# Performance work log

Measured on AMD Instinct MI355X. Metric: run time of the kernel, lower is better.

## Reference

```python
import jax, jax.numpy as jnp
import numpy as np

H = 128

def setup_inputs() -> dict:
    key = jax.random.key(0)
    ks = jax.random.split(key, 7)
    x = jax.random.normal(ks[0], (4, 65536, H), dtype=jnp.float32)
    # Linear(3H -> H) and Linear(H -> H), torch-style fan-in init scale
    W1 = jax.random.normal(ks[1], (3 * H, H), dtype=jnp.float32) / np.sqrt(3 * H)
    b1 = jax.random.normal(ks[2], (H,), dtype=jnp.float32) * 0.01
    W2 = jax.random.normal(ks[3], (H, H), dtype=jnp.float32) / np.sqrt(H)
    b2 = jax.random.normal(ks[4], (H,), dtype=jnp.float32) * 0.01
    gamma = jnp.ones((H,), dtype=jnp.float32)
    beta = jnp.zeros((H,), dtype=jnp.float32)
    return {"x": x, "W1": W1, "b1": b1, "W2": W2, "b2": b2, "gamma": gamma, "beta": beta}


def _layernorm(h, gamma, beta, eps=1e-5):
    mu = jnp.mean(h, axis=-1, keepdims=True)
    var = jnp.var(h, axis=-1, keepdims=True)
    return (h - mu) * jax.lax.rsqrt(var + eps) * gamma + beta


def reference(x, W1, b1, W2, b2, gamma, beta):
    # circular neighbor gather along node dim
    prev_x = jnp.roll(x, 1, axis=1)
    next_x = jnp.roll(x, -1, axis=1)
    cat = jnp.concatenate([prev_x, x, next_x], axis=-1)  # [B, N, 3H]
    h = jax.nn.relu(jnp.einsum('bnc,ch->bnh', cat, W1) + b1)
    delta = jnp.einsum('bnh,hk->bnk', h, W2) + b2
    return jax.nn.relu(_layernorm(x + delta, gamma, beta))
```

## Files before the change

### kernel.cpp

```cpp
#include <hip/hip_runtime.h>


typedef __bf16 bf16x8 __attribute__((ext_vector_type(8)));
typedef __bf16 bf16x4 __attribute__((ext_vector_type(4)));
typedef float  f32x4  __attribute__((ext_vector_type(4)));

#define H      128
#define NB     65536
#define TILE   64
#define XS     136
#define HSS    136
#define VS     132
#define NTILES 4096

__global__ __launch_bounds__(256, 2)
void cbb_kernel(const float* __restrict__ x, const float* __restrict__ W1,
                const float* __restrict__ b1, const float* __restrict__ W2,
                const float* __restrict__ b2, const float* __restrict__ gamma,
                const float* __restrict__ beta, float* __restrict__ out) {
    __shared__ __align__(16) char raw[(66 * XS + 64 * HSS) * 2];
    __bf16* xs = (__bf16*)raw;
    __bf16* hs = xs + 66 * XS;
    float*  vs = (float*)raw;
    __shared__ float s_mu[64], s_rs[64], s_gamma[128], s_beta[128];

    const int tid  = threadIdx.x;
    const int wid  = tid >> 6;
    const int lane = tid & 63;
    const int l    = lane & 15;
    const int g    = lane >> 4;
    const int col0 = wid * 32;
    const int c0   = col0 + l;
    const int c1   = col0 + 16 + l;

    if (tid < 128) { s_gamma[tid] = gamma[tid]; s_beta[tid] = beta[tid]; }

    const float b1r0 = b1[c0], b1r1 = b1[c1];
    const float b2r0 = b2[c0], b2r1 = b2[c1];

    bf16x8 w1f[12][2];
#pragma unroll
    for (int ks = 0; ks < 12; ++ks) {
#pragma unroll
        for (int ct = 0; ct < 2; ++ct) {
            const int cc = col0 + ct * 16 + l;
            bf16x8 f;
#pragma unroll
            for (int j = 0; j < 8; ++j)
                f[j] = (__bf16)W1[(ks * 32 + g * 8 + j) * H + cc];
            w1f[ks][ct] = f;
        }
    }
    bf16x8 w2f[4][2];
#pragma unroll
    for (int ks = 0; ks < 4; ++ks) {
#pragma unroll
        for (int ct = 0; ct < 2; ++ct) {
            const int cc = col0 + ct * 16 + l;
            bf16x8 f;
#pragma unroll
            for (int j = 0; j < 8; ++j)
                f[j] = (__bf16)W2[(ks * 32 + g * 8 + j) * H + cc];
            w2f[ks][ct] = f;
        }
    }

    for (int t = blockIdx.x; t < NTILES; t += gridDim.x) {
        const int b  = t >> 10;
        const int n0 = (t & 1023) << 6;
        const size_t rowbase = (size_t)b * NB;

        __syncthreads();

        for (int q = tid; q < 66 * 32; q += 256) {
            const int r = q >> 5, c = q & 31;
            const int grow = (n0 - 1 + r + NB) & (NB - 1);
            const float4 f = *(const float4*)(x + ((rowbase + grow) * H + c * 4));
            bf16x4 v4;
            v4[0] = (__bf16)f.x; v4[1] = (__bf16)f.y;
            v4[2] = (__bf16)f.z; v4[3] = (__bf16)f.w;
            *(bf16x4*)(xs + r * XS + c * 4) = v4;
        }
        __syncthreads();

        f32x4 acc[4][2];
#pragma unroll
        for (int rt = 0; rt < 4; ++rt)
#pragma unroll
            for (int ct = 0; ct < 2; ++ct)
                acc[rt][ct] = (f32x4){0.f, 0.f, 0.f, 0.f};

#pragma unroll
        for (int rt = 0; rt < 4; ++rt) {
            const int rb = rt * 16 + l;
#pragma unroll
            for (int ks = 0; ks < 12; ++ks) {
                const int k = ks * 32 + g * 8;
                const bf16x8 a = *(const bf16x8*)(xs + (rb + (k >> 7)) * XS + (k & 127));
                acc[rt][0] = __builtin_amdgcn_mfma_f32_16x16x32_bf16(a, w1f[ks][0], acc[rt][0], 0, 0, 0);
                acc[rt][1] = __builtin_amdgcn_mfma_f32_16x16x32_bf16(a, w1f[ks][1], acc[rt][1], 0, 0, 0);
            }
        }

#pragma unroll
        for (int rt = 0; rt < 4; ++rt) {
#pragma unroll
            for (int i = 0; i < 4; ++i) {
                const int row = rt * 16 + g * 4 + i;
                hs[row * HSS + c0] = (__bf16)fmaxf(acc[rt][0][i] + b1r0, 0.f);
                hs[row * HSS + c1] = (__bf16)fmaxf(acc[rt][1][i] + b1r1, 0.f);
            }
        }
        __syncthreads();

        f32x4 acc2[4][2];
#pragma unroll
        for (int rt = 0; rt < 4; ++rt)
#pragma unroll
            for (int ct = 0; ct < 2; ++ct)
                acc2[rt][ct] = (f32x4){0.f, 0.f, 0.f, 0.f};

#pragma unroll
        for (int rt = 0; rt < 4; ++rt) {
            const int rb = rt * 16 + l;
#pragma unroll
            for (int ks = 0; ks < 4; ++ks) {
                const bf16x8 a = *(const bf16x8*)(hs + rb * HSS + ks * 32 + g * 8);
                acc2[rt][0] = __builtin_amdgcn_mfma_f32_16x16x32_bf16(a, w2f[ks][0], acc2[rt][0], 0, 0, 0);
                acc2[rt][1] = __builtin_amdgcn_mfma_f32_16x16x32_bf16(a, w2f[ks][1], acc2[rt][1], 0, 0, 0);
            }
        }

#pragma unroll
        for (int rt = 0; rt < 4; ++rt) {
#pragma unroll
            for (int i = 0; i < 4; ++i) {
                const int row = rt * 16 + g * 4 + i;
                acc2[rt][0][i] += b2r0 + (float)xs[(row + 1) * XS + c0];
                acc2[rt][1][i] += b2r1 + (float)xs[(row + 1) * XS + c1];
            }
        }
        __syncthreads();

#pragma unroll
        for (int rt = 0; rt < 4; ++rt) {
#pragma unroll
            for (int i = 0; i < 4; ++i) {
                const int row = rt * 16 + g * 4 + i;
                vs[row * VS + c0] = acc2[rt][0][i];
                vs[row * VS + c1] = acc2[rt][1][i];
            }
        }
        __syncthreads();

        {
            const int row = tid >> 2;
            const int cb  = (tid & 3) * 32;
            float s = 0.f, qq = 0.f;
#pragma unroll
            for (int c8 = 0; c8 < 8; ++c8) {
                const f32x4 vv = *(const f32x4*)(vs + row * VS + cb + c8 * 4);
#pragma unroll
                for (int e = 0; e < 4; ++e) { s += vv[e]; qq += vv[e] * vv[e]; }
            }
            s  += __shfl_xor(s, 1, 4);  s  += __shfl_xor(s, 2, 4);
            qq += __shfl_xor(qq, 1, 4); qq += __shfl_xor(qq, 2, 4);
            const float muv = s * (1.f / 128.f);
            const float var = qq * (1.f / 128.f) - muv * muv;
            if ((tid & 3) == 0) { s_mu[row] = muv; s_rs[row] = rsqrtf(var + 1e-5f); }
        }
        __syncthreads();

        {
            const int row = tid >> 2;
            const int cb  = (tid & 3) * 32;
            const float muv = s_mu[row], rv = s_rs[row];
            float* op = out + (rowbase + n0 + row) * H + cb;
#pragma unroll
            for (int c8 = 0; c8 < 8; ++c8) {
                const f32x4 vv = *(const f32x4*)(vs + row * VS + cb + c8 * 4);
                const f32x4 gm = *(const f32x4*)(s_gamma + cb + c8 * 4);
                const f32x4 bt = *(const f32x4*)(s_beta + cb + c8 * 4);
                f32x4 o;
#pragma unroll
                for (int e = 0; e < 4; ++e)
                    o[e] = fmaxf((vv[e] - muv) * rv * gm[e] + bt[e], 0.f);
                *(f32x4*)(op + c8 * 4) = o;
            }
        }
    }
}

extern "C" void kernel_launch(void* const* d_in, const int* in_sizes, int n_in,
                              void* d_out, int out_size, void* d_ws, size_t ws_size,
                              hipStream_t stream) {
    const float* x     = (const float*)d_in[0];
    const float* W1    = (const float*)d_in[1];
    const float* b1    = (const float*)d_in[2];
    const float* W2    = (const float*)d_in[3];
    const float* b2    = (const float*)d_in[4];
    const float* gamma = (const float*)d_in[5];
    const float* beta  = (const float*)d_in[6];
    float* out = (float*)d_out;

    cbb_kernel<<<512, 256, 0, stream>>>(x, W1, b1, W2, b2, gamma, beta, out);
}
```

Measured before the change: 296.6 us.

## Restructure kernel into per-wave row chunks with shared-memory weights and register-only epilogue

Weights move from per-thread registers into shared memory, laid out in MFMA fragment order and shared by 16 waves in a 1024-thread block. Each wave now handles 16-row chunks on its own. It computes the transposed product (W as the A operand), reads x directly from global memory with software prefetch, and passes the hidden activations between GEMMs through lane shuffles instead of LDS. LayerNorm is done in registers with cross-lane shuffles, which removes every per-tile __syncthreads and the LDS staging. In exchange, the neighbouring x rows are reloaded from global memory (about 3x reads, likely served by cache), weights are read from LDS on every MFMA, and occupancy is one block per CU.

Result: slower. 998.0 us (+236.5%).

```diff
diff --git a/kernel.cpp b/kernel.cpp
--- a/kernel.cpp
+++ b/kernel.cpp
@@ -2,191 +2,180 @@
 
 
 typedef __bf16 bf16x8 __attribute__((ext_vector_type(8)));
-typedef __bf16 bf16x4 __attribute__((ext_vector_type(4)));
 typedef float  f32x4  __attribute__((ext_vector_type(4)));
 
 #define H      128
 #define NB     65536
-#define TILE   64
-#define XS     136
-#define HSS    136
-#define VS     132
-#define NTILES 4096
+#define BLK    1024
+#define GRID   256
+#define RPW    64
+#define CHUNK  16
 
-__global__ __launch_bounds__(256, 2)
+union U8 { bf16x8 v; unsigned u[4]; };
+
+static __device__ __forceinline__ unsigned pkbf(float a, float b) {
+    union { __bf16 h; unsigned short u; } ua, ub;
+    ua.h = (__bf16)a; ub.h = (__bf16)b;
+    return ((unsigned)ub.u << 16) | (unsigned)ua.u;
+}
+
+__global__ __launch_bounds__(BLK, 1)
 void cbb_kernel(const float* __restrict__ x, const float* __restrict__ W1,
                 const float* __restrict__ b1, const float* __restrict__ W2,
                 const float* __restrict__ b2, const float* __restrict__ gamma,
                 const float* __restrict__ beta, float* __restrict__ out) {
-    __shared__ __align__(16) char raw[(66 * XS + 64 * HSS) * 2];
-    __bf16* xs = (__bf16*)raw;
-    __bf16* hs = xs + 66 * XS;
-    float*  vs = (float*)raw;
-    __shared__ float s_mu[64], s_rs[64], s_gamma[128], s_beta[128];
+    __shared__ __align__(16) __bf16 w1s[12 * 8 * 512];
+    __shared__ __align__(16) __bf16 w2s[4 * 8 * 512];
+    __shared__ __align__(16) float s_b1[128], s_b2[128], s_gamma[128], s_beta[128];
 
     const int tid  = threadIdx.x;
     const int wid  = tid >> 6;
     const int lane = tid & 63;
     const int l    = lane & 15;
     const int g    = lane >> 4;
-    const int col0 = wid * 32;
-    const int c0   = col0 + l;
-    const int c1   = col0 + 16 + l;
 
-    if (tid < 128) { s_gamma[tid] = gamma[tid]; s_beta[tid] = beta[tid]; }
+    if (tid < 128) {
+        s_b1[tid] = b1[tid];       s_b2[tid]   = b2[tid];
+        s_gamma[tid] = gamma[tid]; s_beta[tid] = beta[tid];
+    }
 
-    const float b1r0 = b1[c0], b1r1 = b1[c1];
-    const float b2r0 = b2[c0], b2r1 = b2[c1];
-
-    bf16x8 w1f[12][2];
-#pragma unroll
-    for (int ks = 0; ks < 12; ++ks) {
-#pragma unroll
-        for (int ct = 0; ct < 2; ++ct) {
-            const int cc = col0 + ct * 16 + l;
-            bf16x8 f;
-#pragma unroll
-            for (int j = 0; j < 8; ++j)
-                f[j] = (__bf16)W1[(ks * 32 + g * 8 + j) * H + cc];
-            w1f[ks][ct] = f;
+    for (int idx = tid; idx < 65536; idx += BLK) {
+        const int fid = idx >> 9;
+        const int e   = idx & 511;
+        const int le  = e >> 3, j = e & 7;
+        const int lel = le & 15, leg = le >> 4;
+        if (fid < 96) {
+            const int ks = fid >> 3, cb = fid & 7;
+            w1s[idx] = (__bf16)W1[(ks * 32 + leg * 8 + j) * H + cb * 16 + lel];
+        } else {
+            const int f2 = fid - 96;
+            const int ks = f2 >> 3, cb = f2 & 7;
+            w2s[f2 * 512 + e] = (__bf16)W2[(ks * 32 + leg * 8 + j) * H + cb * 16 + lel];
         }
     }
-    bf16x8 w2f[4][2];
+    __syncthreads();
+
+    const __bf16* w1l = w1s + lane * 8;
+    const __bf16* w2l = w2s + lane * 8;
+
+    const int lA = l + 16 * (2 * (g & 1) + (g >> 1));
+    const int lB = l + 16 * (2 * (g & 1) + 1 - (g >> 1));
+    const bool odd = (g & 1) != 0;
+    const bool hi  = (g >> 1) != 0;
+
+    const int wave_id = blockIdx.x * 16 + wid;
+    const int r0base  = wave_id * RPW;
+
+    for (int c = 0; c < RPW / CHUNK; ++c) {
+        const int r0 = r0base + c * CHUNK;
+        const int bb = r0 >> 16;
+        const int n0 = r0 & (NB - 1);
+        const size_t rowbase = (size_t)bb * NB;
+
+        f32x4 acc[8];
 #pragma unroll
-    for (int ks = 0; ks < 4; ++ks) {
+        for (int cb = 0; cb < 8; ++cb) acc[cb] = (f32x4){0.f, 0.f, 0.f, 0.f};
+
+        float4 la, lb;
+        {
+            const int row = (n0 + l - 1) & (NB - 1);
+            const float* p = x + (rowbase + row) * H + g * 8;
+            la = *(const float4*)p; lb = *(const float4*)(p + 4);
+        }
 #pragma unroll
-        for (int ct = 0; ct < 2; ++ct) {
-            const int cc = col0 + ct * 16 + l;
-            bf16x8 f;
+        for (int ks = 0; ks < 12; ++ks) {
+            float4 na = la, nb2 = lb;
+            if (ks < 11) {
+                const int ks1 = ks + 1;
+                const int row = (n0 + l + (ks1 >> 2) - 1) & (NB - 1);
+                const float* p = x + (rowbase + row) * H + (ks1 & 3) * 32 + g * 8;
+                na = *(const float4*)p; nb2 = *(const float4*)(p + 4);
+            }
+            bf16x8 af;
+            af[0] = (__bf16)la.x; af[1] = (__bf16)la.y;
+            af[2] = (__bf16)la.z; af[3] = (__bf16)la.w;
+            af[4] = (__bf16)lb.x; af[5] = (__bf16)lb.y;
+            af[6] = (__bf16)lb.z; af[7] = (__bf16)lb.w;
 #pragma unroll
-            for (int j = 0; j < 8; ++j)
-                f[j] = (__bf16)W2[(ks * 32 + g * 8 + j) * H + cc];
-            w2f[ks][ct] = f;
+            for (int cb = 0; cb < 8; ++cb) {
+                const bf16x8 wf = *(const bf16x8*)(w1l + (ks * 8 + cb) * 512);
+                acc[cb] = __builtin_amdgcn_mfma_f32_16x16x32_bf16(wf, af, acc[cb], 0, 0, 0);
+            }
+            la = na; lb = nb2;
         }
-    }
 
-    for (int t = blockIdx.x; t < NTILES; t += gridDim.x) {
-        const int b  = t >> 10;
-        const int n0 = (t & 1023) << 6;
-        const size_t rowbase = (size_t)b * NB;
+        unsigned pb[8][2];
+#pragma unroll
+        for (int cb = 0; cb < 8; ++cb) {
+            const f32x4 bq = *(const f32x4*)(s_b1 + cb * 16 + g * 4);
+            const float v0 = fmaxf(acc[cb][0] + bq[0], 0.f);
+            const float v1 = fmaxf(acc[cb][1] + bq[1], 0.f);
+            const float v2 = fmaxf(acc[cb][2] + bq[2], 0.f);
+            const float v3 = fmaxf(acc[cb][3] + bq[3], 0.f);
+            pb[cb][0] = pkbf(v0, v1);
+            pb[cb][1] = pkbf(v2, v3);
+        }
 
-        __syncthreads();
+        bf16x8 pa[4];
+#pragma unroll
+        for (int ks2 = 0; ks2 < 4; ++ks2) {
+            const unsigned sA0 = odd ? pb[2 * ks2 + 1][0] : pb[2 * ks2][0];
+            const unsigned sA1 = odd ? pb[2 * ks2 + 1][1] : pb[2 * ks2][1];
+            const unsigned sB0 = odd ? pb[2 * ks2][0]     : pb[2 * ks2 + 1][0];
+            const unsigned sB1 = odd ? pb[2 * ks2][1]     : pb[2 * ks2 + 1][1];
+            const unsigned a0 = (unsigned)__shfl((int)sA0, lA);
+            const unsigned a1 = (unsigned)__shfl((int)sA1, lA);
+            const unsigned b0 = (unsigned)__shfl((int)sB0, lB);
+            const unsigned b1 = (unsigned)__shfl((int)sB1, lB);
+            U8 t;
+            t.u[0] = hi ? b0 : a0;
+            t.u[1] = hi ? b1 : a1;
+            t.u[2] = hi ? a0 : b0;
+            t.u[3] = hi ? a1 : b1;
+            pa[ks2] = t.v;
+        }
 
-        for (int q = tid; q < 66 * 32; q += 256) {
-            const int r = q >> 5, c = q & 31;
-            const int grow = (n0 - 1 + r + NB) & (NB - 1);
-            const float4 f = *(const float4*)(x + ((rowbase + grow) * H + c * 4));
-            bf16x4 v4;
-            v4[0] = (__bf16)f.x; v4[1] = (__bf16)f.y;
-            v4[2] = (__bf16)f.z; v4[3] = (__bf16)f.w;
-            *(bf16x4*)(xs + r * XS + c * 4) = v4;
-        }
-        __syncthreads();
-
-        f32x4 acc[4][2];
+        f32x4 acc2[8];
 #pragma unroll
-        for (int rt = 0; rt < 4; ++rt)
+        for (int cb = 0; cb < 8; ++cb) acc2[cb] = (f32x4){0.f, 0.f, 0.f, 0.f};
 #pragma unroll
-            for (int ct = 0; ct < 2; ++ct)
-                acc[rt][ct] = (f32x4){0.f, 0.f, 0.f, 0.f};
-
+        for (int ks2 = 0; ks2 < 4; ++ks2) {
 #pragma unroll
-        for (int rt = 0; rt < 4; ++rt) {
-            const int rb = rt * 16 + l;
-#pragma unroll
-            for (int ks = 0; ks < 12; ++ks) {
-                const int k = ks * 32 + g * 8;
-                const bf16x8 a = *(const bf16x8*)(xs + (rb + (k >> 7)) * XS + (k & 127));
-                acc[rt][0] = __builtin_amdgcn_mfma_f32_16x16x32_bf16(a, w1f[ks][0], acc[rt][0], 0, 0, 0);
-                acc[rt][1] = __builtin_amdgcn_mfma_f32_16x16x32_bf16(a, w1f[ks][1], acc[rt][1], 0, 0, 0);
+            for (int cb = 0; cb < 8; ++cb) {
+                const bf16x8 wf = *(const bf16x8*)(w2l + (ks2 * 8 + cb) * 512);
+                acc2[cb] = __builtin_amdgcn_mfma_f32_16x16x32_bf16(wf, pa[ks2], acc2[cb], 0, 0, 0);
             }
         }
 
+        const float* xr = x + (rowbase + n0 + l) * H;
+        float s = 0.f, qq = 0.f;
 #pragma unroll
-        for (int rt = 0; rt < 4; ++rt) {
+        for (int cb = 0; cb < 8; ++cb) {
+            const f32x4 xv = *(const f32x4*)(xr + cb * 16 + g * 4);
+            const f32x4 bq = *(const f32x4*)(s_b2 + cb * 16 + g * 4);
 #pragma unroll
             for (int i = 0; i < 4; ++i) {
-                const int row = rt * 16 + g * 4 + i;
-                hs[row * HSS + c0] = (__bf16)fmaxf(acc[rt][0][i] + b1r0, 0.f);
-                hs[row * HSS + c1] = (__bf16)fmaxf(acc[rt][1][i] + b1r1, 0.f);
+                acc2[cb][i] += bq[i] + xv[i];
+                s  += acc2[cb][i];
+                qq += acc2[cb][i] * acc2[cb][i];
             }
         }
-        __syncthreads();
+        s  += __shfl_xor(s, 16);  s  += __shfl_xor(s, 32);
+        qq += __shfl_xor(qq, 16); qq += __shfl_xor(qq, 32);
+        const float mu = s * (1.f / 128.f);
+        const float var = qq * (1.f / 128.f) - mu * mu;
+        const float rv = rsqrtf(var + 1e-5f);
 
-        f32x4 acc2[4][2];
+        float* op = out + (rowbase + n0 + l) * H;
 #pragma unroll
-        for (int rt = 0; rt < 4; ++rt)
+        for (int cb = 0; cb < 8; ++cb) {
+            const f32x4 gm = *(const f32x4*)(s_gamma + cb * 16 + g * 4);
+            const f32x4 bt = *(const f32x4*)(s_beta + cb * 16 + g * 4);
+            f32x4 o;
 #pragma unroll
-            for (int ct = 0; ct < 2; ++ct)
-                acc2[rt][ct] = (f32x4){0.f, 0.f, 0.f, 0.f};
-
-#pragma unroll
-        for (int rt = 0; rt < 4; ++rt) {
-            const int rb = rt * 16 + l;
-#pragma unroll
-            for (int ks = 0; ks < 4; ++ks) {
-                const bf16x8 a = *(const bf16x8*)(hs + rb * HSS + ks * 32 + g * 8);
-                acc2[rt][0] = __builtin_amdgcn_mfma_f32_16x16x32_bf16(a, w2f[ks][0], acc2[rt][0], 0, 0, 0);
-                acc2[rt][1] = __builtin_amdgcn_mfma_f32_16x16x32_bf16(a, w2f[ks][1], acc2[rt][1], 0, 0, 0);
-            }
-        }
-
-#pragma unroll
-        for (int rt = 0; rt < 4; ++rt) {
-#pragma unroll
-            for (int i = 0; i < 4; ++i) {
-                const int row = rt * 16 + g * 4 + i;
-                acc2[rt][0][i] += b2r0 + (float)xs[(row + 1) * XS + c0];
-                acc2[rt][1][i] += b2r1 + (float)xs[(row + 1) * XS + c1];
-            }
-        }
-        __syncthreads();
-
-#pragma unroll
-        for (int rt = 0; rt < 4; ++rt) {
-#pragma unroll
-            for (int i = 0; i < 4; ++i) {
-                const int row = rt * 16 + g * 4 + i;
-                vs[row * VS + c0] = acc2[rt][0][i];
-                vs[row * VS + c1] = acc2[rt][1][i];
-            }
-        }
-        __syncthreads();
-
-        {
-            const int row = tid >> 2;
-            const int cb  = (tid & 3) * 32;
-            float s = 0.f, qq = 0.f;
-#pragma unroll
-            for (int c8 = 0; c8 < 8; ++c8) {
-                const f32x4 vv = *(const f32x4*)(vs + row * VS + cb + c8 * 4);
-#pragma unroll
-                for (int e = 0; e < 4; ++e) { s += vv[e]; qq += vv[e] * vv[e]; }
-            }
-            s  += __shfl_xor(s, 1, 4);  s  += __shfl_xor(s, 2, 4);
-            qq += __shfl_xor(qq, 1, 4); qq += __shfl_xor(qq, 2, 4);
-            const float muv = s * (1.f / 128.f);
-            const float var = qq * (1.f / 128.f) - muv * muv;
-            if ((tid & 3) == 0) { s_mu[row] = muv; s_rs[row] = rsqrtf(var + 1e-5f); }
-        }
-        __syncthreads();
-
-        {
-            const int row = tid >> 2;
-            const int cb  = (tid & 3) * 32;
-            const float muv = s_mu[row], rv = s_rs[row];
-            float* op = out + (rowbase + n0 + row) * H + cb;
-#pragma unroll
-            for (int c8 = 0; c8 < 8; ++c8) {
-                const f32x4 vv = *(const f32x4*)(vs + row * VS + cb + c8 * 4);
-                const f32x4 gm = *(const f32x4*)(s_gamma + cb + c8 * 4);
-                const f32x4 bt = *(const f32x4*)(s_beta + cb + c8 * 4);
-                f32x4 o;
-#pragma unroll
-                for (int e = 0; e < 4; ++e)
-                    o[e] = fmaxf((vv[e] - muv) * rv * gm[e] + bt[e], 0.f);
-                *(f32x4*)(op + c8 * 4) = o;
-            }
+            for (int i = 0; i < 4; ++i)
+                o[i] = fmaxf((acc2[cb][i] - mu) * rv * gm[i] + bt[i], 0.f);
+            *(f32x4*)(op + cb * 16 + g * 4) = o;
         }
     }
 }
@@ -203,5 +192,5 @@
     const float* beta  = (const float*)d_in[6];
     float* out = (float*)d_out;
 
-    cbb_kernel<<<512, 256, 0, stream>>>(x, W1, b1, W2, b2, gamma, beta, out);
+    cbb_kernel<<<GRID, BLK, 0, stream>>>(x, W1, b1, W2, b2, gamma, beta, out);
 }
```
